# Optimization experiments

Hardware: AMD Instinct MI355X
Metric: run time of the kernel (lower is better)

Reference implementation:

```python
import jax, jax.numpy as jnp
import numpy as np

N_ITER = 50      # fixed number of Sinkhorn iterations (numItermax)
REG = 10.0       # entropic regularization epsilon
TAU = 1000.0     # absorption threshold for log-stabilization


def setup_inputs() -> dict:
    key = jax.random.key(0)
    k1, k2 = jax.random.split(key)
    x = jax.random.normal(k1, (4096, 64), dtype=jnp.float32)
    y = jax.random.normal(k2, (4096, 64), dtype=jnp.float32)
    return {"x": x, "y": y}


def _sinkhorn_loss(x, y):
    n, m = x.shape[0], y.shape[0]
    # squared-euclidean ground cost: ||x_i||^2 + ||y_j||^2 - 2 <x_i, y_j>
    M = (x ** 2).sum(1)[:, None] + (y ** 2).sum(1)[None, :] - 2.0 * (x @ y.T)
    a = jnp.full((n,), 1.0 / n, dtype=x.dtype)  # uniform source marginal
    b = jnp.full((m,), 1.0 / m, dtype=x.dtype)  # uniform target marginal
    eps = jnp.asarray(1e-16, x.dtype)

    def kernel(alpha, beta):
        # log-space stabilized kernel K = exp(-(M - alpha - beta)/reg)
        return jnp.exp(-(M - alpha[:, None] - beta[None, :]) / REG)

    def body(carry, _):
        alpha, beta, u, v = carry
        K = kernel(alpha, beta)
        v = b / (K.T @ u + eps)
        u = a / (K @ v + eps)
        # absorption step: fold large scalings into alpha/beta, reset u,v
        absorb = (jnp.abs(u).max() > TAU) | (jnp.abs(v).max() > TAU)
        alpha = jnp.where(absorb, alpha + REG * jnp.log(u), alpha)
        beta = jnp.where(absorb, beta + REG * jnp.log(v), beta)
        u = jnp.where(absorb, a, u)  # ones/n == a (uniform)
        v = jnp.where(absorb, b, v)  # ones/m == b (uniform)
        return (alpha, beta, u, v), None

    init = (jnp.zeros(n, x.dtype), jnp.zeros(m, x.dtype), a, b)
    (alpha, beta, u, v), _ = jax.lax.scan(jax.checkpoint(body), init, None, length=N_ITER)
    # transport plan Gamma in log space (get_Gamma)
    Gamma = jnp.exp(-(M - alpha[:, None] - beta[None, :]) / REG
                    + jnp.log(u)[:, None] + jnp.log(v)[None, :])
    # Sinkhorn loss <Gamma, M>
    return (Gamma * M).sum()


def reference(x, y):
    return _sinkhorn_loss(x, y)
```

## Files before the change

kernel.cpp:

```cpp
#include <hip/hip_runtime.h>
#include <hip/hip_cooperative_groups.h>

namespace cg = cooperative_groups;

typedef unsigned char u8;
typedef unsigned short u16;
typedef unsigned int u32;

#define NN 4096
#define NITER 50
#define REGE 10.0f
#define AMARG (1.0f / 4096.0f)
#define NB 256
#define KSCL 4096.0f
#define KLN2 8.317766166719343f

__device__ __forceinline__ float wsum(float v) {
#pragma unroll
    for (int off = 32; off; off >>= 1) v += __shfl_xor(v, off, 64);
    return v;
}
__device__ __forceinline__ u8 f2e5(float f) {
    union { _Float16 h; u16 u; } cv; cv.h = (_Float16)f;
    const u16 h = cv.u;
    return (u8)((h + 0x7F + ((h >> 8) & 1)) >> 8);
}
typedef _Float16 h2v __attribute__((ext_vector_type(2)));
__device__ __forceinline__ void dec4(u32 w, float* o) {
    const u32 h01 = __builtin_amdgcn_perm(0u, w, 0x01040004u);
    const u32 h23 = __builtin_amdgcn_perm(0u, w, 0x03040204u);
    const h2v p01 = __builtin_bit_cast(h2v, h01);
    const h2v p23 = __builtin_bit_cast(h2v, h23);
    o[0] = (float)p01.x; o[1] = (float)p01.y;
    o[2] = (float)p23.x; o[3] = (float)p23.y;
}

__device__ __forceinline__ float agent_ldf(const float* p) {
    return __hip_atomic_load(p, __ATOMIC_RELAXED, __HIP_MEMORY_SCOPE_AGENT);
}
__device__ __forceinline__ void agent_stf(float* p, float v) {
    __hip_atomic_store(p, v, __ATOMIC_RELAXED, __HIP_MEMORY_SCOPE_AGENT);
}
__device__ __forceinline__ int agent_ldi(const int* p) {
    return __hip_atomic_load(p, __ATOMIC_RELAXED, __HIP_MEMORY_SCOPE_AGENT);
}

__device__ __forceinline__ void bump(int* ctr, int tid) {
    __syncthreads();
    if (tid == 0) {
        asm volatile("s_waitcnt vmcnt(0)" ::: "memory");
        (void)__hip_atomic_fetch_add(ctr, 1, __ATOMIC_RELAXED, __HIP_MEMORY_SCOPE_AGENT);
    }
}
__device__ __forceinline__ void spin(int* ctr, int target, int tid) {
    if (tid == 0) {
        while (agent_ldi(ctr) < target) __builtin_amdgcn_s_sleep(1);
    }
    __syncthreads();
}

__global__ __launch_bounds__(1024, 4) void sinkhorn_all(
    const float* __restrict__ x, const float* __restrict__ y, float* __restrict__ out,
    u8* __restrict__ K0,
    float* __restrict__ xsq, float* __restrict__ ysq,
    float* __restrict__ tpart, float* __restrict__ spart,
    float* __restrict__ lossacc, int* __restrict__ bar) {
    cg::grid_group grid = cg::this_grid();
    union Sh {
        struct { float xs[64][65]; float ys[64][65]; } bld;
        struct {
            float uts[512];
            float psumA[16][16][9];
            float vtl[128];
            float psh[16];
        } it;
    };
    __shared__ Sh sh;

    const int tid  = threadIdx.x;
    const int lane = tid & 63;
    const int wid  = tid >> 6;
    const int b    = blockIdx.x;
    const int c    = b & 7;
    const int l    = b >> 3;

    int* tpd = bar + l * 16;
    int* spd = bar + 512 + c * 16;
    int* outdone = bar + 640;

    for (int r = b * 16 + wid; r < 2 * NN; r += NB * 16) {
        const float* src = (r < NN) ? (x + (size_t)r * 64) : (y + (size_t)(r - NN) * 64);
        float t = src[lane];
        float s = wsum(t * t);
        if (lane == 0) { if (r < NN) xsq[r] = s; else ysq[r - NN] = s; }
    }
    if (b == 0) {
        if (tid < 656) bar[tid] = 0;
        if (tid == 0) lossacc[0] = 0.f;
    }
    grid.sync();

    {
        const int tx = tid & 31, ty = tid >> 5;
        for (int rt = 0; rt < 8; ++rt) {
            const int i0 = 512 * c + 64 * rt;
            __syncthreads();
            {
                const int row = tid >> 4, col4 = (tid & 15) * 4;
                *(float4*)&sh.bld.xs[row][col4] = *(const float4*)(x + (size_t)(i0 + row) * 64 + col4);
            }
            for (int ct = 0; ct < 2; ++ct) {
                const int j0 = 128 * l + 64 * ct;
                __syncthreads();
                {
                    const int row = tid >> 4, col4 = (tid & 15) * 4;
                    *(float4*)&sh.bld.ys[row][col4] = *(const float4*)(y + (size_t)(j0 + row) * 64 + col4);
                }
                __syncthreads();
                float a00 = 0, a01 = 0, a10 = 0, a11 = 0;
#pragma unroll
                for (int k = 0; k < 64; ++k) {
                    const float x0 = sh.bld.xs[ty * 2][k],     x1 = sh.bld.xs[ty * 2 + 1][k];
                    const float y0 = sh.bld.ys[tx * 2][k],     y1 = sh.bld.ys[tx * 2 + 1][k];
                    a00 = __fmaf_rn(x0, y0, a00); a01 = __fmaf_rn(x0, y1, a01);
                    a10 = __fmaf_rn(x1, y0, a10); a11 = __fmaf_rn(x1, y1, a11);
                }
                const float xq0 = xsq[i0 + ty * 2], xq1 = xsq[i0 + ty * 2 + 1];
                const float yq0 = ysq[j0 + tx * 2], yq1 = ysq[j0 + tx * 2 + 1];
                const float C = 0.14426950408889634f;
                const u8 q00 = f2e5(exp2f(12.f - (xq0 + yq0 - 2.f * a00) * C));
                const u8 q01 = f2e5(exp2f(12.f - (xq0 + yq1 - 2.f * a01) * C));
                const u8 q10 = f2e5(exp2f(12.f - (xq1 + yq0 - 2.f * a10) * C));
                const u8 q11 = f2e5(exp2f(12.f - (xq1 + yq1 - 2.f * a11) * C));
                *(u16*)(K0 + (size_t)(i0 + ty * 2) * NN + j0 + tx * 2)     = (u16)(q00 | (q01 << 8));
                *(u16*)(K0 + (size_t)(i0 + ty * 2 + 1) * NN + j0 + tx * 2) = (u16)(q10 | (q11 << 8));
            }
        }
    }

    for (int n = 0; n < NITER; ++n) {
        const int p = n & 1;

        const int jj = tid & 15, gg = tid >> 4;
        const u8* kbase = K0 + (size_t)(512 * c + 8 * gg) * NN + 128 * l + 8 * jj;
        uint2 kr[8];
#pragma unroll
        for (int ii = 0; ii < 8; ++ii)
            kr[ii] = *(const uint2*)(kbase + (size_t)ii * NN);

        if (n == 0) {
            if (tid < 512) sh.it.uts[tid] = AMARG;
        } else {
            spin(spd, 32 * n, tid);
            const float* sp = spart + (size_t)(((n - 1) & 1) * 8 + c) * 16384;
            const int r = tid >> 1, h = tid & 1;
            float acc = 0.f;
#pragma unroll
            for (int lp = 0; lp < 16; ++lp)
                acc += agent_ldf(sp + (16 * h + lp) * 512 + r);
            acc += __shfl_xor(acc, 1, 64);
            if (h == 0) sh.it.uts[r] = 1.0f / acc;
        }
        __syncthreads();

        {
            float acc[8] = {};
#pragma unroll
            for (int ii = 0; ii < 8; ++ii) {
                const float ui = sh.it.uts[8 * gg + ii];
                float qv[8];
                dec4(kr[ii].x, qv); dec4(kr[ii].y, qv + 4);
#pragma unroll
                for (int k = 0; k < 8; ++k) acc[k] = __fmaf_rn(qv[k], ui, acc[k]);
            }
#pragma unroll
            for (int k = 0; k < 8; ++k) {
                acc[k] += __shfl_xor(acc[k], 16, 64);
                acc[k] += __shfl_xor(acc[k], 32, 64);
            }
            if ((lane >> 4) == 0) {
#pragma unroll
                for (int k = 0; k < 8; ++k) sh.it.psumA[wid][lane][k] = acc[k];
            }
        }
        __syncthreads();
        if (tid < 128) {
            float tot = 0.f;
#pragma unroll
            for (int w = 0; w < 16; ++w) tot += sh.it.psumA[w][tid >> 3][tid & 7];
            agent_stf(tpart + (size_t)(p * 8 + c) * 4096 + 128 * l + tid, tot);
        }

        const int r = tid >> 1, h = tid & 1;
        const u8* kb = K0 + (size_t)(512 * c + r) * NN + 128 * l + 64 * h;
        uint4 kq[4];
#pragma unroll
        for (int s4 = 0; s4 < 4; ++s4)
            kq[s4] = *(const uint4*)(kb + s4 * 16);

        bump(tpd, tid);
        spin(tpd, 8 * (n + 1), tid);
        if (tid < 128) {
            const float* tb = tpart + (size_t)p * 32768 + 128 * l + tid;
            float tq = 0.f;
#pragma unroll
            for (int cc = 0; cc < 8; ++cc) tq += agent_ldf(tb + cc * 4096);
            sh.it.vtl[tid] = 1.0f / tq;
        }
        __syncthreads();

        {
            float s = 0.f;
#pragma unroll
            for (int s4 = 0; s4 < 4; ++s4) {
                float qv[16];
                dec4(kq[s4].x, qv);      dec4(kq[s4].y, qv + 4);
                dec4(kq[s4].z, qv + 8);  dec4(kq[s4].w, qv + 12);
                const float* vp = &sh.it.vtl[64 * h + s4 * 16];
#pragma unroll
                for (int k = 0; k < 16; ++k) s = __fmaf_rn(qv[k], vp[k], s);
            }
            s += __shfl_xor(s, 1, 64);
            if (h == 0)
                agent_stf(spart + (size_t)(p * 8 + c) * 16384 + l * 512 + r, s);
        }
        bump(spd, tid);
    }

    spin(spd, 32 * NITER, tid);
    {
        const float* sp = spart + (size_t)(((NITER - 1) & 1) * 8 + c) * 16384;
        const int r = tid >> 1, h = tid & 1;
        float acc = 0.f;
#pragma unroll
        for (int lp = 0; lp < 16; ++lp)
            acc += agent_ldf(sp + (16 * h + lp) * 512 + r);
        acc += __shfl_xor(acc, 1, 64);
        if (h == 0) sh.it.uts[r] = 1.0f / acc;
    }
    __syncthreads();
    {
        const int r = tid >> 1, h = tid & 1;
        const u8* kb = K0 + (size_t)(512 * c + r) * NN + 128 * l + 64 * h;
        uint4 kq[4];
#pragma unroll
        for (int s4 = 0; s4 < 4; ++s4)
            kq[s4] = *(const uint4*)(kb + s4 * 16);
        float a1 = 0.f, a2 = 0.f;
#pragma unroll
        for (int s4 = 0; s4 < 4; ++s4) {
            float qv[16];
            dec4(kq[s4].x, qv);      dec4(kq[s4].y, qv + 4);
            dec4(kq[s4].z, qv + 8);  dec4(kq[s4].w, qv + 12);
            const float* vp = &sh.it.vtl[64 * h + s4 * 16];
#pragma unroll
            for (int k = 0; k < 16; ++k) {
                const float q = qv[k];
                a2 = __fmaf_rn(q, vp[k], a2);
                a1 = __fmaf_rn(q * __logf(fmaxf(q, 1e-30f)), vp[k], a1);
            }
        }
        a1 += __shfl_xor(a1, 1, 64);
        a2 += __shfl_xor(a2, 1, 64);
        float rowv = (h == 0) ? (a1 - KLN2 * a2) * sh.it.uts[r] : 0.f;
        rowv = wsum(rowv);
        if (lane == 0) sh.it.psh[wid] = rowv;
    }
    __syncthreads();
    if (tid == 0) {
        float bacc = 0.f;
#pragma unroll
        for (int w = 0; w < 16; ++w) bacc += sh.it.psh[w];
        (void)__hip_atomic_fetch_add(lossacc, bacc, __ATOMIC_RELAXED,
                                     __HIP_MEMORY_SCOPE_AGENT);
        asm volatile("s_waitcnt vmcnt(0)" ::: "memory");
        const int old = __hip_atomic_fetch_add(outdone, 1,
                                               __ATOMIC_RELAXED, __HIP_MEMORY_SCOPE_AGENT);
        if (old == NB - 1)
            agent_stf(out, agent_ldf(lossacc) * (-REGE / KSCL));
    }
}

extern "C" void kernel_launch(void* const* d_in, const int* in_sizes, int n_in,
                              void* d_out, int out_size, void* d_ws, size_t ws_size,
                              hipStream_t stream) {
    const float* x = (const float*)d_in[0];
    const float* y = (const float*)d_in[1];
    float* out = (float*)d_out;
    char* ws = (char*)d_ws;

    u8* K0 = (u8*)(ws);
    float* xsq = (float*)(ws + 16777216ull);
    float* ysq = xsq + 4096;
    float* tpart = ysq + 4096;
    float* spart = tpart + 65536;
    float* lossacc = spart + 262144;
    int* bar = (int*)(lossacc + 16);

    void* args[] = {&x, &y, &out, &K0, &xsq, &ysq, &tpart, &spart, &lossacc, &bar};

    hipError_t err = hipLaunchCooperativeKernel((void*)sinkhorn_all, dim3(NB), dim3(1024),
                                                (void**)args, 0, stream);
    if (err != hipSuccess)
        (void)hipLaunchCooperativeKernel((void*)sinkhorn_all, dim3(NB), dim3(1024),
                                         (void**)args, 0, stream);
}
```

Baseline: 783.4 us.

## Replace atomic counter barriers with per-block flag arrays and tagged loss slots

Swaps the atomic fetch-add counters used for inter-block synchronisation for per-producer flag words. Each block stores its iteration number into its own flag and consumers poll the minimum over 8 or 32 flags. The final loss reduction no longer uses float atomics and a done counter. Each block instead writes a tagged 64-bit value, and block 0 polls and sums all 256 slots, which also makes the sum order deterministic. This is meant to cut contention on shared atomic counters, at the cost of more polling loads per spin and a serial 256-slot scan in block 0.

```diff
diff --git a/kernel.cpp b/kernel.cpp
--- a/kernel.cpp
+++ b/kernel.cpp
@@ -6,6 +6,7 @@
 typedef unsigned char u8;
 typedef unsigned short u16;
 typedef unsigned int u32;
+typedef unsigned long long u64;
 
 #define NN 4096
 #define NITER 50
@@ -44,17 +45,38 @@
 __device__ __forceinline__ int agent_ldi(const int* p) {
     return __hip_atomic_load(p, __ATOMIC_RELAXED, __HIP_MEMORY_SCOPE_AGENT);
 }
-
-__device__ __forceinline__ void bump(int* ctr, int tid) {
+__device__ __forceinline__ void agent_sti(int* p, int v) {
+    __hip_atomic_store(p, v, __ATOMIC_RELAXED, __HIP_MEMORY_SCOPE_AGENT);
+}
+__device__ __forceinline__ u64 agent_ld64(const u64* p) {
+    return __hip_atomic_load(p, __ATOMIC_RELAXED, __HIP_MEMORY_SCOPE_AGENT);
+}
+__device__ __forceinline__ void agent_st64(u64* p, u64 v) {
+    __hip_atomic_store(p, v, __ATOMIC_RELAXED, __HIP_MEMORY_SCOPE_AGENT);
+}
+__device__ __forceinline__ u64 pk(float v, u32 tag) {
+    return ((u64)tag << 32) | (u64)__float_as_uint(v);
+}
+__device__ __forceinline__ float upv(u64 w) { return __uint_as_float((u32)w); }
+__device__ __forceinline__ u32 uptag(u64 w) { return (u32)(w >> 32); }
+
+__device__ __forceinline__ void publish(int* f, int v, int tid) {
     __syncthreads();
     if (tid == 0) {
         asm volatile("s_waitcnt vmcnt(0)" ::: "memory");
-        (void)__hip_atomic_fetch_add(ctr, 1, __ATOMIC_RELAXED, __HIP_MEMORY_SCOPE_AGENT);
-    }
-}
-__device__ __forceinline__ void spin(int* ctr, int target, int tid) {
+        agent_sti(f, v);
+    }
+}
+template <int N>
+__device__ __forceinline__ void pollN(const int* f, int target, int tid) {
     if (tid == 0) {
-        while (agent_ldi(ctr) < target) __builtin_amdgcn_s_sleep(1);
+        for (;;) {
+            int mn = 0x7fffffff;
+#pragma unroll
+            for (int i = 0; i < N; ++i) mn = min(mn, agent_ldi(f + i));
+            if (mn >= target) break;
+            __builtin_amdgcn_s_sleep(1);
+        }
     }
     __syncthreads();
 }
@@ -64,7 +86,7 @@
     u8* __restrict__ K0,
     float* __restrict__ xsq, float* __restrict__ ysq,
     float* __restrict__ tpart, float* __restrict__ spart,
-    float* __restrict__ lossacc, int* __restrict__ bar) {
+    u64* __restrict__ lossq, int* __restrict__ bar) {
     cg::grid_group grid = cg::this_grid();
     union Sh {
         struct { float xs[64][65]; float ys[64][65]; } bld;
@@ -84,9 +106,8 @@
     const int c    = b & 7;
     const int l    = b >> 3;
 
-    int* tpd = bar + l * 16;
-    int* spd = bar + 512 + c * 16;
-    int* outdone = bar + 640;
+    int* tpf = bar + l * 8;
+    int* spf = bar + 256 + c * 32;
 
     for (int r = b * 16 + wid; r < 2 * NN; r += NB * 16) {
         const float* src = (r < NN) ? (x + (size_t)r * 64) : (y + (size_t)(r - NN) * 64);
@@ -94,10 +115,8 @@
         float s = wsum(t * t);
         if (lane == 0) { if (r < NN) xsq[r] = s; else ysq[r - NN] = s; }
     }
-    if (b == 0) {
-        if (tid < 656) bar[tid] = 0;
-        if (tid == 0) lossacc[0] = 0.f;
-    }
+    if (b == 0 && tid < 512) bar[tid] = 0;
+    if (tid == 0) lossq[b] = 0ull;
     grid.sync();
 
     {
@@ -150,8 +169,9 @@
 
         if (n == 0) {
             if (tid < 512) sh.it.uts[tid] = AMARG;
+            __syncthreads();
         } else {
-            spin(spd, 32 * n, tid);
+            pollN<32>(spf, n, tid);
             const float* sp = spart + (size_t)(((n - 1) & 1) * 8 + c) * 16384;
             const int r = tid >> 1, h = tid & 1;
             float acc = 0.f;
@@ -160,8 +180,8 @@
                 acc += agent_ldf(sp + (16 * h + lp) * 512 + r);
             acc += __shfl_xor(acc, 1, 64);
             if (h == 0) sh.it.uts[r] = 1.0f / acc;
-        }
-        __syncthreads();
+            __syncthreads();
+        }
 
         {
             float acc[8] = {};
@@ -198,8 +218,8 @@
         for (int s4 = 0; s4 < 4; ++s4)
             kq[s4] = *(const uint4*)(kb + s4 * 16);
 
-        bump(tpd, tid);
-        spin(tpd, 8 * (n + 1), tid);
+        publish(tpf + c, n + 1, tid);
+        pollN<8>(tpf, n + 1, tid);
         if (tid < 128) {
             const float* tb = tpart + (size_t)p * 32768 + 128 * l + tid;
             float tq = 0.f;
@@ -224,10 +244,10 @@
             if (h == 0)
                 agent_stf(spart + (size_t)(p * 8 + c) * 16384 + l * 512 + r, s);
         }
-        bump(spd, tid);
-    }
-
-    spin(spd, 32 * NITER, tid);
+        publish(spf + l, n + 1, tid);
+    }
+
+    pollN<32>(spf, NITER, tid);
     {
         const float* sp = spart + (size_t)(((NITER - 1) & 1) * 8 + c) * 16384;
         const int r = tid >> 1, h = tid & 1;
@@ -271,13 +291,22 @@
         float bacc = 0.f;
 #pragma unroll
         for (int w = 0; w < 16; ++w) bacc += sh.it.psh[w];
-        (void)__hip_atomic_fetch_add(lossacc, bacc, __ATOMIC_RELAXED,
-                                     __HIP_MEMORY_SCOPE_AGENT);
-        asm volatile("s_waitcnt vmcnt(0)" ::: "memory");
-        const int old = __hip_atomic_fetch_add(outdone, 1,
-                                               __ATOMIC_RELAXED, __HIP_MEMORY_SCOPE_AGENT);
-        if (old == NB - 1)
-            agent_stf(out, agent_ldf(lossacc) * (-REGE / KSCL));
+        agent_st64(lossq + b, pk(bacc, 1u));
+        if (b == 0) {
+            float tot;
+            for (;;) {
+                bool ok = true;
+                float s = 0.f;
+                for (int i = 0; i < NB; ++i) {
+                    const u64 v = agent_ld64(lossq + i);
+                    ok &= (uptag(v) == 1u);
+                    s += upv(v);
+                }
+                if (ok) { tot = s; break; }
+                __builtin_amdgcn_s_sleep(1);
+            }
+            agent_stf(out, tot * (-REGE / KSCL));
+        }
     }
 }
 
@@ -294,10 +323,10 @@
     float* ysq = xsq + 4096;
     float* tpart = ysq + 4096;
     float* spart = tpart + 65536;
-    float* lossacc = spart + 262144;
-    int* bar = (int*)(lossacc + 16);
-
-    void* args[] = {&x, &y, &out, &K0, &xsq, &ysq, &tpart, &spart, &lossacc, &bar};
+    u64* lossq = (u64*)(spart + 262144);
+    int* bar = (int*)(lossq + 256);
+
+    void* args[] = {&x, &y, &out, &K0, &xsq, &ysq, &tpart, &spart, &lossq, &bar};
 
     hipError_t err = hipLaunchCooperativeKernel((void*)sinkhorn_all, dim3(NB), dim3(1024),
                                                 (void**)args, 0, stream);
```

Result: slower. 829.1 us (+5.8%).
